# Performance work log

Measured on AMD Instinct MI355X. Metric: run time of the kernel, lower is better.

## Reference

```python
import jax, jax.numpy as jnp
import numpy as np

EPS = 1e-4


def setup_inputs() -> dict:
    key = jax.random.key(0)
    k1, k2, k3, k4, k5 = jax.random.split(key, 5)
    N, M, F = 2048, 2048, 128
    embeds = jax.random.uniform(k1, (N, F), dtype=jnp.float32)
    base_embeds = jax.random.normal(k2, (M, F), dtype=jnp.float32)
    base_rewards = jax.random.normal(k3, (M,), dtype=jnp.float32)
    # torch Linear(num_feat, num_feat, bias=False) / Linear(num_feat, 1, bias=False)
    # stored here as [in, out] for x @ W convention
    W1 = jax.random.normal(k4, (F, F), dtype=jnp.float32) / np.sqrt(F)
    w2 = jax.random.normal(k5, (F, 1), dtype=jnp.float32) / np.sqrt(F)
    return {"embeds": embeds, "base_embeds": base_embeds,
            "base_rewards": base_rewards, "W1": W1, "w2": w2}


def reference(embeds, base_embeds, base_rewards, W1, w2):
    # pairwise differences: [N, M, F]
    diff = embeds[:, None, :] - base_embeds[None, :, :]
    # tiny MLP distance kernel: Linear -> ELU -> Linear, abs
    h = jax.nn.elu(jnp.einsum('nmf,fg->nmg', diff, W1))
    dist = jnp.abs(jnp.einsum('nmg,go->nmo', h, w2)[:, :, 0])  # [N, M]
    # inverse-distance normalized weights
    dist_w = 1.0 / (dist + EPS)
    dist_w = dist_w / jnp.sum(dist_w, axis=1, keepdims=True)
    rewards = jnp.sum(dist_w * base_rewards[None, :], axis=1)  # [N]
    return rewards
```

## Files before the change

kernel.cpp:

```cpp
#include <hip/hip_runtime.h>
#include <hip/hip_bf16.h>

#define F      128
#define NROWS  2048
#define MROWS  2048
#define BN     128
#define BM     64
#define MT     (MROWS/BM)
#define LOG2E  1.44269504088896340736f

typedef float f32x2 __attribute__((ext_vector_type(2)));
typedef float f32x4 __attribute__((ext_vector_type(4)));

__device__ __forceinline__ f32x2 lo2(f32x4 v) { return __builtin_shufflevector(v, v, 0, 1); }
__device__ __forceinline__ f32x2 hi2(f32x4 v) { return __builtin_shufflevector(v, v, 2, 3); }
__device__ __forceinline__ f32x2 pk_add(f32x2 a, f32x2 b) {
    f32x2 d; asm("v_pk_add_f32 %0, %1, %2" : "=v"(d) : "v"(a), "v"(b)); return d;
}
__device__ __forceinline__ f32x2 pk_mul(f32x2 a, f32x2 b) {
    f32x2 d; asm("v_pk_mul_f32 %0, %1, %2" : "=v"(d) : "v"(a), "v"(b)); return d;
}
__device__ __forceinline__ void gload16(const float* g, float* l) {
    __builtin_amdgcn_global_load_lds(
        (const __attribute__((address_space(1))) void*)g,
        (__attribute__((address_space(3))) void*)l, 16, 0, 0);
}

__global__ __launch_bounds__(256) void proj_kernel(
    const float* __restrict__ embeds, const float* __restrict__ base,
    const float* __restrict__ W1, const float* __restrict__ w2,
    float* __restrict__ PA, float* __restrict__ PB,
    float* __restrict__ w2sum)
{
    const int tid = threadIdx.x;
    const int sub = tid >> 7;
    const int g   = tid & 127;
    const int row = blockIdx.x * 2 + sub;

    __shared__ float xs[2][F];
    {
        const float* src = (row < NROWS) ? &embeds[(size_t)row * F]
                                         : &base[(size_t)(row - NROWS) * F];
        xs[sub][g] = src[g];
    }
    __syncthreads();

    float acc = 0.0f;
#pragma unroll 8
    for (int f = 0; f < F; ++f)
        acc = fmaf(xs[sub][f], W1[f * F + g], acc);

    const float wv = w2[g];
    const int   ch = g >> 4, go = g & 15;
    if (row < NROWS) {
        float* dst = PA + (size_t)row * 256 + ch * 32 + go;
        dst[0]  = (acc + 1.0f) * wv;
        dst[16] = __builtin_amdgcn_exp2f(acc * LOG2E) * wv;
    } else {
        float* dst = PB + (size_t)(row - NROWS) * 256 + ch * 32 + go;
        dst[0]  = -acc * wv;
        dst[16] = __builtin_amdgcn_exp2f(-acc * LOG2E);
    }

    if (blockIdx.x == 0 && tid < 64) {
        float s = w2[tid] + w2[tid + 64];
#pragma unroll
        for (int k = 1; k < 64; k <<= 1) s += __shfl_xor(s, k);
        if (tid == 0) *w2sum = s;
    }
}

__global__ __launch_bounds__(256, 3) void pair_kernel(
    const float* __restrict__ PA, const float* __restrict__ PB,
    const float* __restrict__ w2, const float* __restrict__ w2sum_p,
    const float* __restrict__ brew, float* __restrict__ partials)
{
    __shared__ float sbuf[2][6144];
    __shared__ float w2l[F];

    const int tid = threadIdx.x;
    const int w    = tid >> 6;
    const int l    = tid & 63;
    const int nt   = blockIdx.x, mt = blockIdx.y;
    const int n0   = nt * BN,    m0 = mt * BM;
    const int tr   = tid >> 4,   tc = tid & 15;
    const int fa   = (tr & 7) * 4,  fb = (tc & 7) * 4;
    const int rsub = l >> 3;
    const int lswz = 4 * ((l & 7) ^ rsub);

#define STAGE(CH, BUF) {                                                        \
    const float* pa = PA + (size_t)(n0 + rsub) * 256 + (CH) * 32 + lswz;        \
    _Pragma("unroll")                                                           \
    for (int t = 0; t < 4; ++t) {                                               \
        const int k = t * 4 + w;                                                \
        gload16(pa + (size_t)(8 * k) * 256, &sbuf[BUF][k * 256]);               \
    }                                                                           \
    const float* pb = PB + (size_t)(m0 + rsub) * 256 + (CH) * 32 + lswz;        \
    _Pragma("unroll")                                                           \
    for (int t = 0; t < 2; ++t) {                                               \
        const int k = t * 4 + w;                                                \
        gload16(pb + (size_t)(8 * k) * 256, &sbuf[BUF][4096 + k * 256]);        \
    } }

    f32x2 acc2[8][2];
#pragma unroll
    for (int i = 0; i < 8; ++i)
#pragma unroll
        for (int jj = 0; jj < 2; ++jj) acc2[i][jj] = (f32x2)(0.0f);

    STAGE(0, 0)
    if (tid < F) w2l[tid] = w2[tid];
    __syncthreads();

#pragma unroll 1
    for (int ch = 0; ch < 8; ++ch) {
        const int buf = ch & 1;
        if (ch < 7) STAGE(ch + 1, buf ^ 1);

        const float* sb = sbuf[buf];
#pragma unroll
        for (int g4 = 0; g4 < 16; g4 += 4) {
            const f32x4 wq = *(const f32x4*)&w2l[ch * 16 + g4];
            f32x4 b1v[4], bev[4];
#pragma unroll
            for (int j = 0; j < 4; ++j) {
                const float* bb = sb + 4096 + (tc + 16 * j) * 32;
                b1v[j] = *(const f32x4*)&bb[g4 ^ fb];
                bev[j] = *(const f32x4*)&bb[(16 + g4) ^ fb];
            }
#pragma unroll
            for (int i = 0; i < 8; ++i) {
                const float* ab = sb + (tr + 16 * i) * 32;
                const f32x4 a1 = *(const f32x4*)&ab[g4 ^ fa];
                const f32x4 ae = *(const f32x4*)&ab[(16 + g4) ^ fa];
                const f32x2 a1l = lo2(a1), a1h = hi2(a1);
                const f32x2 ael = lo2(ae), aeh = hi2(ae);
#pragma unroll
                for (int jj = 0; jj < 2; ++jj) {
                    const f32x2 xl0 = pk_add(a1l, lo2(b1v[2 * jj]));
                    const f32x2 xh0 = pk_add(a1h, hi2(b1v[2 * jj]));
                    const f32x2 el0 = pk_mul(ael, lo2(bev[2 * jj]));
                    const f32x2 eh0 = pk_mul(aeh, hi2(bev[2 * jj]));
                    const f32x2 xl1 = pk_add(a1l, lo2(b1v[2 * jj + 1]));
                    const f32x2 xh1 = pk_add(a1h, hi2(b1v[2 * jj + 1]));
                    const f32x2 el1 = pk_mul(ael, lo2(bev[2 * jj + 1]));
                    const f32x2 eh1 = pk_mul(aeh, hi2(bev[2 * jj + 1]));
                    f32x2 s0, s1, s2, s3;
                    s0.x = __builtin_amdgcn_fmed3f(xl0.x, el0.x, wq.x);
                    s0.y = __builtin_amdgcn_fmed3f(xl1.x, el1.x, wq.x);
                    s1.x = __builtin_amdgcn_fmed3f(xl0.y, el0.y, wq.y);
                    s1.y = __builtin_amdgcn_fmed3f(xl1.y, el1.y, wq.y);
                    s2.x = __builtin_amdgcn_fmed3f(xh0.x, eh0.x, wq.z);
                    s2.y = __builtin_amdgcn_fmed3f(xh1.x, eh1.x, wq.z);
                    s3.x = __builtin_amdgcn_fmed3f(xh0.y, eh0.y, wq.w);
                    s3.y = __builtin_amdgcn_fmed3f(xh1.y, eh1.y, wq.w);
                    f32x2 t = acc2[i][jj];
                    t = pk_add(t, s0);
                    t = pk_add(t, s1);
                    t = pk_add(t, s2);
                    t = pk_add(t, s3);
                    acc2[i][jj] = t;
                }
            }
        }
        __syncthreads();
    }
#undef STAGE

    const float w2sum = *w2sum_p;
    float rsv[4];
#pragma unroll
    for (int j = 0; j < 4; ++j) rsv[j] = brew[m0 + tc + 16 * j];

#pragma unroll
    for (int i = 0; i < 8; ++i) {
        float sw = 0.0f, swr = 0.0f;
#pragma unroll
        for (int j = 0; j < 4; ++j) {
            const float tot  = (j & 1) ? acc2[i][j >> 1].y : acc2[i][j >> 1].x;
            const float dist = fabsf(tot - w2sum);
            const float wgt  = 1.0f / (dist + 1e-4f);
            sw += wgt;
            swr = fmaf(wgt, rsv[j], swr);
        }
#pragma unroll
        for (int k = 1; k < 16; k <<= 1) {
            sw  += __shfl_xor(sw, k);
            swr += __shfl_xor(swr, k);
        }
        if (tc == 0) {
            const int n = n0 + tr + 16 * i;
            partials[((size_t)n * MT + mt) * 2 + 0] = sw;
            partials[((size_t)n * MT + mt) * 2 + 1] = swr;
        }
    }
}

__global__ __launch_bounds__(256) void finalize_kernel(
    const float* __restrict__ partials, float* __restrict__ out)
{
    const int n = blockIdx.x * 256 + threadIdx.x;
    if (n < NROWS) {
        float sw = 0.0f, swr = 0.0f;
#pragma unroll
        for (int t = 0; t < MT; ++t) {
            sw  += partials[((size_t)n * MT + t) * 2 + 0];
            swr += partials[((size_t)n * MT + t) * 2 + 1];
        }
        out[n] = swr / sw;
    }
}

extern "C" void kernel_launch(void* const* d_in, const int* in_sizes, int n_in,
                              void* d_out, int out_size, void* d_ws, size_t ws_size,
                              hipStream_t stream)
{
    const float* embeds       = (const float*)d_in[0];
    const float* base_embeds  = (const float*)d_in[1];
    const float* base_rewards = (const float*)d_in[2];
    const float* W1           = (const float*)d_in[3];
    const float* w2           = (const float*)d_in[4];
    float* out = (float*)d_out;

    float* partials = (float*)d_ws;
    float* PA  = partials + (size_t)NROWS * MT * 2;
    float* PB  = PA + (size_t)NROWS * 256;
    float* w2s = PB + (size_t)MROWS * 256;

    proj_kernel<<<(NROWS + MROWS) / 2, 256, 0, stream>>>(
        embeds, base_embeds, W1, w2, PA, PB, w2s);

    dim3 grid2(NROWS / BN, MROWS / BM);
    pair_kernel<<<grid2, 256, 0, stream>>>(PA, PB, w2, w2s, base_rewards, partials);

    finalize_kernel<<<(NROWS + 255) / 256, 256, 0, stream>>>(partials, out);
}
```

Measured before the change: 74.94 us.

## Use padded 20-float LDS rows with 16 chunks and feature-paired accumulators

The precompute output layout changes to 8-feature chunks of 16 floats, and the pair kernel now stages 16 smaller chunks into padded LDS rows of 20 floats instead of XOR-swizzled 32-float rows. This removes bank conflicts without swizzle index math. The inner loop accumulates pairs of features per m-column, using 8x4 f32x2 accumulators that are summed at the end, and feeds med3 from packed results more directly. Launch bounds drop to 2 waves per EU to make room for the doubled accumulator registers, so occupancy is lower and the number of barriers and stages per block doubles.

```diff
diff --git a/kernel.cpp b/kernel.cpp
--- a/kernel.cpp
+++ b/kernel.cpp
@@ -7,7 +7,13 @@
 #define BN     128
 #define BM     64
 #define MT     (MROWS/BM)
+#define NCH    16
 #define LOG2E  1.44269504088896340736f
+
+#define ROWF       20
+#define AB_FLOATS  (BN * ROWF)
+#define BB_FLOATS  (BM * ROWF)
+#define BUF_FLOATS (AB_FLOATS + BB_FLOATS)
 
 typedef float f32x2 __attribute__((ext_vector_type(2)));
 typedef float f32x4 __attribute__((ext_vector_type(4)));
@@ -51,15 +57,15 @@
         acc = fmaf(xs[sub][f], W1[f * F + g], acc);
 
     const float wv = w2[g];
-    const int   ch = g >> 4, go = g & 15;
+    const int   ch = g >> 3, o = g & 7;
     if (row < NROWS) {
-        float* dst = PA + (size_t)row * 256 + ch * 32 + go;
-        dst[0]  = (acc + 1.0f) * wv;
-        dst[16] = __builtin_amdgcn_exp2f(acc * LOG2E) * wv;
+        float* dst = PA + (size_t)row * 256 + ch * 16 + o;
+        dst[0] = (acc + 1.0f) * wv;
+        dst[8] = __builtin_amdgcn_exp2f(acc * LOG2E) * wv;
     } else {
-        float* dst = PB + (size_t)(row - NROWS) * 256 + ch * 32 + go;
-        dst[0]  = -acc * wv;
-        dst[16] = __builtin_amdgcn_exp2f(-acc * LOG2E);
+        float* dst = PB + (size_t)(row - NROWS) * 256 + ch * 16 + o;
+        dst[0] = -acc * wv;
+        dst[8] = __builtin_amdgcn_exp2f(-acc * LOG2E);
     }
 
     if (blockIdx.x == 0 && tid < 64) {
@@ -70,96 +76,92 @@
     }
 }
 
-__global__ __launch_bounds__(256, 3) void pair_kernel(
+__global__ __launch_bounds__(256, 2) void pair_kernel(
     const float* __restrict__ PA, const float* __restrict__ PB,
     const float* __restrict__ w2, const float* __restrict__ w2sum_p,
     const float* __restrict__ brew, float* __restrict__ partials)
 {
-    __shared__ float sbuf[2][6144];
+    __shared__ float sbuf[2 * BUF_FLOATS];
     __shared__ float w2l[F];
 
     const int tid = threadIdx.x;
-    const int w    = tid >> 6;
-    const int l    = tid & 63;
-    const int nt   = blockIdx.x, mt = blockIdx.y;
-    const int n0   = nt * BN,    m0 = mt * BM;
-    const int tr   = tid >> 4,   tc = tid & 15;
-    const int fa   = (tr & 7) * 4,  fb = (tc & 7) * 4;
-    const int rsub = l >> 3;
-    const int lswz = 4 * ((l & 7) ^ rsub);
-
-#define STAGE(CH, BUF) {                                                        \
-    const float* pa = PA + (size_t)(n0 + rsub) * 256 + (CH) * 32 + lswz;        \
-    _Pragma("unroll")                                                           \
-    for (int t = 0; t < 4; ++t) {                                               \
-        const int k = t * 4 + w;                                                \
-        gload16(pa + (size_t)(8 * k) * 256, &sbuf[BUF][k * 256]);               \
-    }                                                                           \
-    const float* pb = PB + (size_t)(m0 + rsub) * 256 + (CH) * 32 + lswz;        \
-    _Pragma("unroll")                                                           \
-    for (int t = 0; t < 2; ++t) {                                               \
-        const int k = t * 4 + w;                                                \
-        gload16(pb + (size_t)(8 * k) * 256, &sbuf[BUF][4096 + k * 256]);        \
-    } }
-
-    f32x2 acc2[8][2];
+    const int wvi = tid >> 6, l = tid & 63;
+    const int nt  = blockIdx.x, mt = blockIdx.y;
+    const int n0  = nt * BN,    m0 = mt * BM;
+    const int tr  = tid >> 4,   tc = tid & 15;
+
+    const float* ssrc[4];
+    int sdst[4];
+#pragma unroll
+    for (int t = 0; t < 4; ++t) {
+        const int k = wvi + 4 * t;
+        int slot, dstf;
+        const float* basep;
+        if (k < 10) { slot = 64 * k + l;        dstf = k * 256;                    basep = PA + (size_t)n0 * 256; }
+        else        { slot = 64 * (k - 10) + l; dstf = AB_FLOATS + (k - 10) * 256; basep = PB + (size_t)m0 * 256; }
+        const int row = slot / 5;
+        const int rs  = slot - row * 5;
+        const int rsd = (rs == 4) ? 0 : rs;
+        ssrc[t] = basep + row * 256 + rsd * 4;
+        sdst[t] = dstf;
+    }
+    const bool has3 = (wvi < 3);
+
+#define STAGE(CH, BUF) {                                                       \
+    gload16(ssrc[0] + (CH) * 16, &sbuf[(BUF) * BUF_FLOATS + sdst[0]]);         \
+    gload16(ssrc[1] + (CH) * 16, &sbuf[(BUF) * BUF_FLOATS + sdst[1]]);         \
+    gload16(ssrc[2] + (CH) * 16, &sbuf[(BUF) * BUF_FLOATS + sdst[2]]);         \
+    if (has3)                                                                   \
+        gload16(ssrc[3] + (CH) * 16, &sbuf[(BUF) * BUF_FLOATS + sdst[3]]); }
+
+    f32x2 acc2[8][4];
 #pragma unroll
     for (int i = 0; i < 8; ++i)
 #pragma unroll
-        for (int jj = 0; jj < 2; ++jj) acc2[i][jj] = (f32x2)(0.0f);
+        for (int j = 0; j < 4; ++j) acc2[i][j] = (f32x2)(0.0f);
 
     STAGE(0, 0)
     if (tid < F) w2l[tid] = w2[tid];
     __syncthreads();
 
 #pragma unroll 1
-    for (int ch = 0; ch < 8; ++ch) {
+    for (int ch = 0; ch < NCH; ++ch) {
         const int buf = ch & 1;
-        if (ch < 7) STAGE(ch + 1, buf ^ 1);
-
-        const float* sb = sbuf[buf];
-#pragma unroll
-        for (int g4 = 0; g4 < 16; g4 += 4) {
-            const f32x4 wq = *(const f32x4*)&w2l[ch * 16 + g4];
+        if (ch + 1 < NCH) STAGE(ch + 1, buf ^ 1)
+
+        const float* sa  = &sbuf[buf * BUF_FLOATS];
+        const float* sbb = sa + AB_FLOATS;
+
+#pragma unroll
+        for (int h = 0; h < 2; ++h) {
+            const f32x2 wlo = *(const f32x2*)&w2l[ch * 8 + h * 4];
+            const f32x2 whi = *(const f32x2*)&w2l[ch * 8 + h * 4 + 2];
             f32x4 b1v[4], bev[4];
 #pragma unroll
             for (int j = 0; j < 4; ++j) {
-                const float* bb = sb + 4096 + (tc + 16 * j) * 32;
-                b1v[j] = *(const f32x4*)&bb[g4 ^ fb];
-                bev[j] = *(const f32x4*)&bb[(16 + g4) ^ fb];
+                const float* bp = sbb + (tc + 16 * j) * ROWF + h * 4;
+                b1v[j] = *(const f32x4*)bp;
+                bev[j] = *(const f32x4*)(bp + 8);
             }
 #pragma unroll
             for (int i = 0; i < 8; ++i) {
-                const float* ab = sb + (tr + 16 * i) * 32;
-                const f32x4 a1 = *(const f32x4*)&ab[g4 ^ fa];
-                const f32x4 ae = *(const f32x4*)&ab[(16 + g4) ^ fa];
+                const float* ap = sa + (tr + 16 * i) * ROWF + h * 4;
+                const f32x4 a1 = *(const f32x4*)ap;
+                const f32x4 ae = *(const f32x4*)(ap + 8);
                 const f32x2 a1l = lo2(a1), a1h = hi2(a1);
                 const f32x2 ael = lo2(ae), aeh = hi2(ae);
 #pragma unroll
-                for (int jj = 0; jj < 2; ++jj) {
-                    const f32x2 xl0 = pk_add(a1l, lo2(b1v[2 * jj]));
-                    const f32x2 xh0 = pk_add(a1h, hi2(b1v[2 * jj]));
-                    const f32x2 el0 = pk_mul(ael, lo2(bev[2 * jj]));
-                    const f32x2 eh0 = pk_mul(aeh, hi2(bev[2 * jj]));
-                    const f32x2 xl1 = pk_add(a1l, lo2(b1v[2 * jj + 1]));
-                    const f32x2 xh1 = pk_add(a1h, hi2(b1v[2 * jj + 1]));
-                    const f32x2 el1 = pk_mul(ael, lo2(bev[2 * jj + 1]));
-                    const f32x2 eh1 = pk_mul(aeh, hi2(bev[2 * jj + 1]));
-                    f32x2 s0, s1, s2, s3;
-                    s0.x = __builtin_amdgcn_fmed3f(xl0.x, el0.x, wq.x);
-                    s0.y = __builtin_amdgcn_fmed3f(xl1.x, el1.x, wq.x);
-                    s1.x = __builtin_amdgcn_fmed3f(xl0.y, el0.y, wq.y);
-                    s1.y = __builtin_amdgcn_fmed3f(xl1.y, el1.y, wq.y);
-                    s2.x = __builtin_amdgcn_fmed3f(xh0.x, eh0.x, wq.z);
-                    s2.y = __builtin_amdgcn_fmed3f(xh1.x, eh1.x, wq.z);
-                    s3.x = __builtin_amdgcn_fmed3f(xh0.y, eh0.y, wq.w);
-                    s3.y = __builtin_amdgcn_fmed3f(xh1.y, eh1.y, wq.w);
-                    f32x2 t = acc2[i][jj];
-                    t = pk_add(t, s0);
-                    t = pk_add(t, s1);
-                    t = pk_add(t, s2);
-                    t = pk_add(t, s3);
-                    acc2[i][jj] = t;
+                for (int j = 0; j < 4; ++j) {
+                    const f32x2 xl = pk_add(a1l, lo2(b1v[j]));
+                    const f32x2 el = pk_mul(ael, lo2(bev[j]));
+                    const f32x2 xh = pk_add(a1h, hi2(b1v[j]));
+                    const f32x2 eh = pk_mul(aeh, hi2(bev[j]));
+                    f32x2 sl, sh;
+                    sl.x = __builtin_amdgcn_fmed3f(xl.x, el.x, wlo.x);
+                    sl.y = __builtin_amdgcn_fmed3f(xl.y, el.y, wlo.y);
+                    sh.x = __builtin_amdgcn_fmed3f(xh.x, eh.x, whi.x);
+                    sh.y = __builtin_amdgcn_fmed3f(xh.y, eh.y, whi.y);
+                    acc2[i][j] = pk_add(acc2[i][j], pk_add(sl, sh));
                 }
             }
         }
@@ -177,7 +179,7 @@
         float sw = 0.0f, swr = 0.0f;
 #pragma unroll
         for (int j = 0; j < 4; ++j) {
-            const float tot  = (j & 1) ? acc2[i][j >> 1].y : acc2[i][j >> 1].x;
+            const float tot  = acc2[i][j].x + acc2[i][j].y;
             const float dist = fabsf(tot - w2sum);
             const float wgt  = 1.0f / (dist + 1e-4f);
             sw += wgt;
```

After: 75.05 us. About the same (+0.1%).
